# Performance work log

Hardware: AMD Instinct MI355X
Metric: run time of the kernel (lower is better)

The kernel has to match this reference:

```python
import jax, jax.numpy as jnp
import numpy as np
from jax import lax

B, CIN, HC, D, H, W = 4, 16, 16, 31, 128, 128


def setup_inputs() -> dict:
    key = jax.random.key(0)
    k1, k2, k3, k4, k5 = jax.random.split(key, 5)
    inputs = jax.random.normal(k1, (B, CIN, D, H, W), dtype=jnp.float32)
    # Conv3d weight: [out=2*HC, in=CIN, 3,3,3]
    conv_w = jax.random.normal(k2, (2 * HC, CIN, 3, 3, 3), dtype=jnp.float32) * 0.05
    # FFN weights stored as [in, out] (equivalent to torch Linear weight.T)
    w1 = jax.random.normal(k3, (HC, 2 * HC), dtype=jnp.float32) * 0.1
    w2 = jax.random.normal(k4, (2 * HC, HC), dtype=jnp.float32) * 0.1
    w3 = jax.random.normal(k5, (HC, 2 * HC), dtype=jnp.float32) * 0.1
    return {"inputs": inputs, "conv_w": conv_w, "w1": w1, "w2": w2, "w3": w3,
            "reverse": 0}


def reference(inputs, conv_w, w1, w2, w3, reverse):
    hc = conv_w.shape[0] // 2
    # 3D conv producing 2*hc gate channels  [B, 2hc, D, H, W]
    gates = lax.conv_general_dilated(
        inputs, conv_w, window_strides=(1, 1, 1), padding='SAME',
        dimension_numbers=('NCDHW', 'OIDHW', 'NCDHW'))
    Z = jnp.tanh(gates[:, :hc])            # [B, hc, D, H, W]
    F = jax.nn.sigmoid(gates[:, hc:])
    # scan over depth (spectral) dim; h0 = 0 reproduces h = (1-f)*z at step 0
    Zs = jnp.moveaxis(Z, 2, 0)             # [D, B, hc, H, W]
    Fs = jnp.moveaxis(F, 2, 0)
    if reverse:
        Zs, Fs = Zs[::-1], Fs[::-1]

    def step(h, zf):
        z, f = zf
        h = f * h + (1.0 - f) * z
        return h, h

    h0 = jnp.zeros_like(Zs[0])
    _, hs = lax.scan(step, h0, (Zs, Fs))   # [D, B, hc, H, W]
    if reverse:
        hs = hs[::-1]
    out = jnp.moveaxis(hs, 0, 2)           # [B, hc, D, H, W]
    # channel-enhanced FFN on channel-last layout
    x = jnp.moveaxis(out, 1, -1)           # [B, D, H, W, hc]
    x1 = jnp.dot(jax.nn.gelu(jnp.dot(x, w1), approximate=False), w2)
    g = jnp.dot(x, w3)                     # [B, D, H, W, 2hc]
    a, wg = jnp.split(g, 2, axis=-1)
    y = x1 + a * jax.nn.sigmoid(wg)
    return jnp.moveaxis(y, -1, 1)          # [B, hc, D, H, W]
```

## Files before the change

### kernel.cpp

```cpp
#include <hip/hip_runtime.h>
#include <hip/hip_fp16.h>

#define HC 16
#define CIN 16
#define BD 31
#define HH 128
#define WW 128
#define PLANE (HH*WW)
#define CH_STRIDE (BD*PLANE)

typedef __attribute__((ext_vector_type(8))) short bf16x8;
typedef __attribute__((ext_vector_type(16))) float f32x16;

__device__ __forceinline__ float sigmoid_fast(float x) {
    return __builtin_amdgcn_rcpf(1.0f + __expf(-x));
}
__device__ __forceinline__ ushort f2bf(float f) {
    unsigned u = __float_as_uint(f);
    u = (u + 0x7fffu + ((u >> 16) & 1u)) >> 16;
    return (ushort)u;
}
__device__ __forceinline__ unsigned pack_bf2(float lo, float hi) {
    unsigned r;
    asm("v_cvt_pk_bf16_f32 %0, %1, %2" : "=v"(r) : "v"(lo), "v"(hi));
    return r;
}
__device__ __forceinline__ float2 sigmoid2(float a, float b) {
    float ea = __expf(-a);
    float eb = __expf(-b);
    float pa = 1.0f + ea, pb = 1.0f + eb;
    float r  = __builtin_amdgcn_rcpf(pa * pb);
    return make_float2(pb * r, pa * r);
}
__device__ __forceinline__ float2 gelu2(float x, float y) {
    float ux = fmaf(0.044715f * x, x * x, x);
    float uy = fmaf(0.044715f * y, y * y, y);
    float ex = __expf(-1.5957691f * ux);
    float ey = __expf(-1.5957691f * uy);
    float px = 1.0f + ex, py = 1.0f + ey;
    float r  = __builtin_amdgcn_rcpf(px * py);
    return make_float2(x * py * r, y * px * r);
}

__global__ void wprep_all(const float* __restrict__ cw,
                          const float* __restrict__ w1,
                          const float* __restrict__ w2,
                          const float* __restrict__ w3,
                          ushort* __restrict__ wtab,
                          ushort* __restrict__ wtab2)
{
    int idx = blockIdx.x * 256 + threadIdx.x;
    if (idx < 13824) {
        int j    = idx & 7;
        int lane = (idx >> 3) & 63;
        int t    = (idx >> 9) % 9;
        int kd   = (idx >> 9) / 9;
        int co = lane & 31;
        int ci = 8 * (lane >> 5) + j;
        int kh = t / 3, kw = t % 3;
        wtab[idx] = f2bf(cw[(co * CIN + ci) * 27 + kd * 9 + kh * 3 + kw]);
        return;
    }
    idx -= 13824;
    if (idx >= 2048) return;
    int e    = idx & 7;
    int lane = (idx >> 3) & 63;
    int tbl  = idx >> 9;
    int m  = lane & 31;
    int hi = lane >> 5;
    int k  = (e & 3) + 8 * (e >> 2) + 4 * hi;
    float v = 0.f;
    if (tbl == 0)      v = w1[k * 32 + m];
    else if (tbl == 3) v = w3[k * 32 + m];
    else {
        int mf = tbl - 1;
        if (m < 16) v = w2[(k + 16 * mf) * 16 + m];
    }
    wtab2[idx] = f2bf(v);
}

__global__ __launch_bounds__(256)
void xprep_kernel(const float* __restrict__ inp, char* __restrict__ xT)
{
    __shared__ float tile[16][256];
    int t  = threadIdx.x;
    int hp = blockIdx.x & 63;
    int g  = blockIdx.x >> 6;
    int d  = g % BD;
    int b  = g / BD;

    size_t src = (size_t)b * CIN * CH_STRIDE + (size_t)d * PLANE + hp * 256;
    #pragma unroll
    for (int c = 0; c < 16; ++c)
        tile[c][t] = inp[src + (size_t)c * CH_STRIDE + t];
    __syncthreads();

    int w  = t & 127;
    int rr = t >> 7;
    char* rowp = xT + (((size_t)(b * BD + d) * 128) + hp * 2 + rr) * 4096;
    #pragma unroll
    for (int q = 0; q < 2; ++q) {
        uint4 pk;
        pk.x = (unsigned)f2bf(tile[q*8+0][t]) | ((unsigned)f2bf(tile[q*8+1][t]) << 16);
        pk.y = (unsigned)f2bf(tile[q*8+2][t]) | ((unsigned)f2bf(tile[q*8+3][t]) << 16);
        pk.z = (unsigned)f2bf(tile[q*8+4][t]) | ((unsigned)f2bf(tile[q*8+5][t]) << 16);
        pk.w = (unsigned)f2bf(tile[q*8+6][t]) | ((unsigned)f2bf(tile[q*8+7][t]) << 16);
        unsigned off = ((unsigned)((w + 1) * 32 + q * 16) ^ (((unsigned)(w + 1) & 0xE) << 3)) - 32;
        *(uint4*)(rowp + off) = pk;
    }
}

#define SLOT_B (3 * 4224)

__device__ __forceinline__ void gload_lds16(const void* g, void* l) {
    __builtin_amdgcn_global_load_lds(
        (const __attribute__((address_space(1))) unsigned int*)g,
        (__attribute__((address_space(3))) unsigned int*)l, 16, 0, 0);
}

__global__ __launch_bounds__(256, 2)
void qrnn_fused(const char* __restrict__ xT,
                const ushort* __restrict__ wtab,
                const ushort* __restrict__ wtab2,
                float* __restrict__ out,
                const int* __restrict__ rev_p)
{
    __shared__ __align__(16) char slab[4][SLOT_B];

    int p = blockIdx.x;
    int logical = (p & 7) * 64 + (p >> 3);
    int b  = logical >> 7;
    int ht = logical & 127;
    int rev = rev_p[0];

    int lane = threadIdx.x & 63;
    int wid  = threadIdx.x >> 6;
    int wl   = lane & 31;
    int hi   = lane >> 5;
    int cio  = hi * 16;

    const bf16x8* wt = (const bf16x8*)wtab;
    bf16x8 af[27];
    #pragma unroll
    for (int t = 0; t < 27; ++t) af[t] = wt[t * 64 + lane];

    const bf16x8* W2 = (const bf16x8*)wtab2;
    bf16x8 af1  = W2[lane];
    bf16x8 af2a = W2[64 + lane];
    bf16x8 af2b = W2[128 + lane];
    bf16x8 af3  = W2[192 + lane];

    unsigned bpo[3];
    #pragma unroll
    for (int dwn = 0; dwn < 3; ++dwn) {
        unsigned wc = (unsigned)(wl + dwn);
        bpo[dwn] = (unsigned)(wid * 1024) + ((wc * 32 + cio) ^ ((wc & 0xE) << 3));
    }

    for (int i = threadIdx.x; i < 4 * 3 * 32; i += 256) {
        int s = i / 96;
        int r = (i / 32) % 3;
        int k = i & 31;
        int off = (k < 8) ? (k * 4) : (4128 + (k - 8) * 4);
        *(int*)(slab[s] + r * 4224 + off) = 0;
    }

    auto zero_slot = [&](int s) {
        for (int i = threadIdx.x; i < 768; i += 256) {
            int r = i >> 8;
            int k = i & 255;
            *(uint4*)(slab[s] + r * 4224 + 32 + k * 16) = uint4{0, 0, 0, 0};
        }
    };

    auto stage = [&](int s, int plane) {
        const char* pl = xT + ((size_t)(b * BD + plane) * 128) * 4096;
        for (int c = wid; c < 12; c += 4) {
            int rr = c >> 2, ch = c & 3;
            int h = ht - 1 + rr;
            char* dst = slab[s] + rr * 4224 + 32 + ch * 1024;
            if ((unsigned)h < (unsigned)HH)
                gload_lds16(pl + (size_t)h * 4096 + ch * 1024 + lane * 16, dst);
            else
                *(uint4*)(dst + lane * 16) = uint4{0, 0, 0, 0};
        }
    };

    f32x16 zacc;
    #pragma unroll
    for (int r = 0; r < 16; ++r) zacc[r] = 0.f;

    auto convd = [&](int d) -> f32x16 {
        f32x16 A = zacc;
        #pragma unroll
        for (int kd = 0; kd < 3; ++kd) {
            const char* sb = slab[(d - 1 + kd) & 3];
            #pragma unroll
            for (int t = 0; t < 9; ++t) {
                bf16x8 bfr = *(const bf16x8*)(sb + (t / 3) * 4224 + bpo[t % 3]);
                A = __builtin_amdgcn_mfma_f32_32x32x16_bf16(af[kd * 9 + t], bfr, A, 0, 0, 0);
            }
        }
        return A;
    };

    float h[8];
    #pragma unroll
    for (int j = 0; j < 8; ++j) h[j] = 0.f;

    float* obase = out + (size_t)b * HC * CH_STRIDE + ht * WW + wid * 32 + wl;

    auto tail = [&](const f32x16& A, int d) {
        union { bf16x8 v; unsigned u[4]; } bx;
        #pragma unroll
        for (int r = 0; r < 8; ++r) {
            float2 s = sigmoid2(2.0f * A[r], A[r + 8]);
            float z = fmaf(2.0f, s.x, -1.0f);
            float f = s.y;
            h[r] = z + f * (h[r] - z);
        }
        #pragma unroll
        for (int q = 0; q < 4; ++q)
            bx.u[q] = pack_bf2(h[2 * q], h[2 * q + 1]);

        f32x16 a1 = __builtin_amdgcn_mfma_f32_32x32x16_bf16(af1, bx.v, zacc, 0, 0, 0);
        f32x16 a3 = __builtin_amdgcn_mfma_f32_32x32x16_bf16(af3, bx.v, zacc, 0, 0, 0);

        union { bf16x8 v; unsigned u[4]; } b2a, b2b;
        #pragma unroll
        for (int q = 0; q < 4; ++q) {
            float2 ga = gelu2(a1[2 * q],     a1[2 * q + 1]);
            float2 gb = gelu2(a1[8 + 2 * q], a1[8 + 2 * q + 1]);
            b2a.u[q] = pack_bf2(ga.x, ga.y);
            b2b.u[q] = pack_bf2(gb.x, gb.y);
        }
        f32x16 a2 = __builtin_amdgcn_mfma_f32_32x32x16_bf16(af2a, b2a.v, zacc, 0, 0, 0);
        a2 = __builtin_amdgcn_mfma_f32_32x32x16_bf16(af2b, b2b.v, a2, 0, 0, 0);

        float* ob = obase + (size_t)d * PLANE;
        #pragma unroll
        for (int q = 0; q < 4; ++q) {
            float2 s = sigmoid2(a3[8 + 2 * q], a3[9 + 2 * q]);
            int c0 = (2 * q     & 3) + 8 * (2 * q     >> 2) + 4 * hi;
            int c1 = (2 * q + 1 & 3) + 8 * (2 * q + 1 >> 2) + 4 * hi;
            ob[(size_t)c0 * CH_STRIDE] = fmaf(a3[2 * q],     s.x, a2[2 * q]);
            ob[(size_t)c1 * CH_STRIDE] = fmaf(a3[2 * q + 1], s.y, a2[2 * q + 1]);
        }
    };

    int d0  = rev ? (BD - 1) : 0;
    int sgn = rev ? -1 : 1;
    int oobq = rev ? -1 : BD;

    stage(d0 & 3, d0);
    stage((d0 + sgn) & 3, d0 + sgn);
    zero_slot((d0 - sgn) & 3);
    __syncthreads();

    f32x16 accP;
    {
        int q = d0 + 2 * sgn;
        if (q >= 0 && q < BD) stage(q & 3, q);
        accP = convd(d0);
        __syncthreads();
    }

    #pragma unroll 1
    for (int i = 1; i < BD; ++i) {
        int d = d0 + sgn * i;
        int q = d + 2 * sgn;
        if (q >= 0 && q < BD) stage(q & 3, q);
        else if (q == oobq)   zero_slot(q & 3);

        f32x16 acc = convd(d);
        tail(accP, d - sgn);
        accP = acc;

        __syncthreads();
    }
    tail(accP, d0 + sgn * (BD - 1));
}

extern "C" void kernel_launch(void* const* d_in, const int* in_sizes, int n_in,
                              void* d_out, int out_size, void* d_ws, size_t ws_size,
                              hipStream_t stream)
{
    const float* inp = (const float*)d_in[0];
    const float* cw  = (const float*)d_in[1];
    const float* w1  = (const float*)d_in[2];
    const float* w2  = (const float*)d_in[3];
    const float* w3  = (const float*)d_in[4];
    const int*   rev = (const int*)d_in[5];

    ushort* wtab  = (ushort*)d_ws;
    ushort* wtab2 = (ushort*)((char*)d_ws + 27648);
    char*   xT    = (char*)d_ws + 32768;

    wprep_all<<<dim3(62), dim3(256), 0, stream>>>(cw, w1, w2, w3, wtab, wtab2);

    xprep_kernel<<<dim3(7936), dim3(256), 0, stream>>>(inp, xT);

    qrnn_fused<<<dim3(512), dim3(256), 0, stream>>>(
        xT, wtab, wtab2, (float*)d_out, rev);
}
```

Before: 135.2 us.

## Reuse each staged depth plane across three rotating conv accumulators

```diff
diff --git a/kernel.cpp b/kernel.cpp
--- a/kernel.cpp
+++ b/kernel.cpp
@@ -12,9 +12,6 @@
 typedef __attribute__((ext_vector_type(8))) short bf16x8;
 typedef __attribute__((ext_vector_type(16))) float f32x16;
 
-__device__ __forceinline__ float sigmoid_fast(float x) {
-    return __builtin_amdgcn_rcpf(1.0f + __expf(-x));
-}
 __device__ __forceinline__ ushort f2bf(float f) {
     unsigned u = __float_as_uint(f);
     u = (u + 0x7fffu + ((u >> 16) & 1u)) >> 16;
@@ -132,6 +129,8 @@
     int b  = logical >> 7;
     int ht = logical & 127;
     int rev = rev_p[0];
+    int sgn = rev ? -1 : 1;
+    int d0  = rev ? (BD - 1) : 0;
 
     int lane = threadIdx.x & 63;
     int wid  = threadIdx.x >> 6;
@@ -140,9 +139,15 @@
     int cio  = hi * 16;
 
     const bf16x8* wt = (const bf16x8*)wtab;
-    bf16x8 af[27];
-    #pragma unroll
-    for (int t = 0; t < 27; ++t) af[t] = wt[t * 64 + lane];
+    int kdA = rev ? 0 : 2;
+    int kdC = rev ? 2 : 0;
+    bf16x8 afA[9], afB[9], afC[9];
+    #pragma unroll
+    for (int t = 0; t < 9; ++t) {
+        afA[t] = wt[(kdA * 9 + t) * 64 + lane];
+        afB[t] = wt[(9      + t) * 64 + lane];
+        afC[t] = wt[(kdC * 9 + t) * 64 + lane];
+    }
 
     const bf16x8* W2 = (const bf16x8*)wtab2;
     bf16x8 af1  = W2[lane];
@@ -165,20 +170,13 @@
         *(int*)(slab[s] + r * 4224 + off) = 0;
     }
 
-    auto zero_slot = [&](int s) {
-        for (int i = threadIdx.x; i < 768; i += 256) {
-            int r = i >> 8;
-            int k = i & 255;
-            *(uint4*)(slab[s] + r * 4224 + 32 + k * 16) = uint4{0, 0, 0, 0};
-        }
-    };
-
-    auto stage = [&](int s, int plane) {
+    auto stage = [&](int plane) {
         const char* pl = xT + ((size_t)(b * BD + plane) * 128) * 4096;
+        char* sb = slab[plane & 3];
         for (int c = wid; c < 12; c += 4) {
             int rr = c >> 2, ch = c & 3;
             int h = ht - 1 + rr;
-            char* dst = slab[s] + rr * 4224 + 32 + ch * 1024;
+            char* dst = sb + rr * 4224 + 32 + ch * 1024;
             if ((unsigned)h < (unsigned)HH)
                 gload_lds16(pl + (size_t)h * 4096 + ch * 1024 + lane * 16, dst);
             else
@@ -189,20 +187,6 @@
     f32x16 zacc;
     #pragma unroll
     for (int r = 0; r < 16; ++r) zacc[r] = 0.f;
-
-    auto convd = [&](int d) -> f32x16 {
-        f32x16 A = zacc;
-        #pragma unroll
-        for (int kd = 0; kd < 3; ++kd) {
-            const char* sb = slab[(d - 1 + kd) & 3];
-            #pragma unroll
-            for (int t = 0; t < 9; ++t) {
-                bf16x8 bfr = *(const bf16x8*)(sb + (t / 3) * 4224 + bpo[t % 3]);
-                A = __builtin_amdgcn_mfma_f32_32x32x16_bf16(af[kd * 9 + t], bfr, A, 0, 0, 0);
-            }
-        }
-        return A;
-    };
 
     float h[8];
     #pragma unroll
@@ -248,37 +232,36 @@
         }
     };
 
-    int d0  = rev ? (BD - 1) : 0;
-    int sgn = rev ? -1 : 1;
-    int oobq = rev ? -1 : BD;
-
-    stage(d0 & 3, d0);
-    stage((d0 + sgn) & 3, d0 + sgn);
-    zero_slot((d0 - sgn) & 3);
+    auto step = [&](int i, f32x16& X, f32x16& Y, f32x16& Z) {
+        if (i > BD) return;
+        int q = d0 + sgn * i;
+        if (i + 2 < BD) stage(d0 + sgn * (i + 2));
+        if (i < BD) {
+            const char* sb = slab[q & 3];
+            #pragma unroll
+            for (int t = 0; t < 9; ++t) {
+                bf16x8 B = *(const bf16x8*)(sb + (t / 3) * 4224 + bpo[t % 3]);
+                X = __builtin_amdgcn_mfma_f32_32x32x16_bf16(afA[t], B, X, 0, 0, 0);
+                Y = __builtin_amdgcn_mfma_f32_32x32x16_bf16(afB[t], B, Y, 0, 0, 0);
+                Z = __builtin_amdgcn_mfma_f32_32x32x16_bf16(afC[t], B, Z, 0, 0, 0);
+            }
+        }
+        if (i >= 1) tail(X, q - sgn);
+        X = zacc;
+        __syncthreads();
+    };
+
+    stage(d0);
+    stage(d0 + sgn);
     __syncthreads();
 
-    f32x16 accP;
-    {
-        int q = d0 + 2 * sgn;
-        if (q >= 0 && q < BD) stage(q & 3, q);
-        accP = convd(d0);
-        __syncthreads();
-    }
-
+    f32x16 accA = zacc, accB = zacc, accC = zacc;
     #pragma unroll 1
-    for (int i = 1; i < BD; ++i) {
-        int d = d0 + sgn * i;
-        int q = d + 2 * sgn;
-        if (q >= 0 && q < BD) stage(q & 3, q);
-        else if (q == oobq)   zero_slot(q & 3);
-
-        f32x16 acc = convd(d);
-        tail(accP, d - sgn);
-        accP = acc;
-
-        __syncthreads();
-    }
-    tail(accP, d0 + sgn * (BD - 1));
+    for (int i = 0; i <= BD; i += 3) {
+        step(i,     accA, accB, accC);
+        step(i + 1, accB, accC, accA);
+        step(i + 2, accC, accA, accB);
+    }
 }
 
 extern "C" void kernel_launch(void* const* d_in, const int* in_sizes, int n_in,
```

After: 132.9 us. About the same (-1.7%).
